# Kernel tuning notes

Measured on AMD Instinct MI355X. Metric: run time of the kernel, lower is better.

Reference implementation:

```python
import jax, jax.numpy as jnp
import numpy as np

N = 50000      # nodes
E = 800000     # edges
R = 8          # relation types
IN = 128       # in_dim
OUT = 128      # out_dim
H = 8          # num_heads
HD = OUT // H  # head dim = 16


def setup_inputs() -> dict:
    key = jax.random.key(0)
    ks = jax.random.split(key, 6)
    return {
        "h": jax.random.normal(ks[0], (N, IN), dtype=jnp.float32),
        "fc_weight": jax.random.normal(ks[1], (R, IN, OUT), dtype=jnp.float32) * 0.05,
        "attn_weight": jax.random.normal(ks[2], (R, H, 2 * HD), dtype=jnp.float32) * 0.05,
        "src": jax.random.randint(ks[3], (E,), 0, N, dtype=jnp.int32),
        "dst": jax.random.randint(ks[4], (E,), 0, N, dtype=jnp.int32),
        "etype": jax.random.randint(ks[5], (E,), 0, R, dtype=jnp.int32),
    }


def reference(h, fc_weight, attn_weight, src, dst, etype):
    # Per-relation projection of ALL node features (equivalent math to the
    # per-edge gathered bmm in the original, without materializing E x IN x OUT):
    # [R, N, OUT] -> [R, N, H, HD]
    z_nodes = jnp.einsum('ni,rio->rno', h, fc_weight).reshape(R, N, H, HD)
    z_s = z_nodes[etype, src]   # [E, H, HD]  (== bmm(h[src], fc_weight[etype]))
    z_d = z_nodes[etype, dst]   # [E, H, HD]
    aw = attn_weight[etype]     # [E, H, 2*HD]
    # a = sum(cat([z_s, z_d], -1) * attn_weight[etype], -1)
    a = jnp.sum(z_s * aw[:, :, :HD], axis=2) + jnp.sum(z_d * aw[:, :, HD:], axis=2)  # [E, H]
    e = jax.nn.leaky_relu(a)    # torch F.leaky_relu_ default slope 0.01

    # Edge softmax per destination node (per head), numerically stable.
    m = jax.ops.segment_max(e, dst, num_segments=N)          # [N, H]
    m = jnp.where(jnp.isfinite(m), m, jnp.zeros_like(m))     # guard empty nodes
    ex = jnp.exp(e - m[dst])                                 # [E, H]
    denom = jax.ops.segment_sum(ex, dst, num_segments=N)     # [N, H]
    num = jax.ops.segment_sum(ex[:, :, None] * z_s, dst, num_segments=N)  # [N, H, HD]
    out = num / jnp.maximum(denom, 1e-9)[:, :, None]         # [N, H, HD]
    return out
```

## Files before the change

kernel.cpp:

```cpp
#include <hip/hip_runtime.h>

#define NN 50000
#define NE 800000
#define NR 8
#define DIN 128
#define DOUT 128
#define NH 8

#define NB_SCAN ((NN + 255) / 256)

typedef __attribute__((ext_vector_type(8))) short bf16x8;
typedef __attribute__((ext_vector_type(4))) float f32x4;

__device__ __forceinline__ unsigned short f2bf(float f) {
  unsigned u = __float_as_uint(f);
  unsigned r = (u + 0x7FFFu + ((u >> 16) & 1u)) >> 16;
  return (unsigned short)r;
}
__device__ __forceinline__ float bf2f(unsigned short b) {
  return __uint_as_float(((unsigned)b) << 16);
}

__global__ __launch_bounds__(256) void prep_fcf(
    const float* __restrict__ fc, const float* __restrict__ attn,
    unsigned short* __restrict__ fcf) {
  int idx = blockIdx.x * 256 + threadIdx.x;
  if (idx >= NR * DIN * 144) return;
  int r = idx / (DIN * 144);
  int rem = idx - r * (DIN * 144);
  int k = rem / 144;
  int j = rem - k * 144;
  float v;
  if (j < DOUT) {
    v = fc[((size_t)r * DIN + k) * DOUT + j];
  } else {
    int cc = j - DOUT;
    int hh = cc & 7, p = cc >> 3;
    const float* fr = fc + ((size_t)r * DIN + k) * DOUT + hh * 16;
    const float* ar = attn + ((size_t)r * NH + hh) * 32 + p * 16;
    v = 0.f;
#pragma unroll
    for (int d = 0; d < 16; ++d) v += fr[d] * ar[d];
  }
  int t = j >> 4, c = j & 15, ks = k >> 5, gg = (k >> 3) & 3, i = k & 7;
  fcf[((((size_t)r * 9 + t) * 4 + ks) * 4 + gg) * 128 + c * 8 + i] = f2bf(v);
}

__global__ __launch_bounds__(256) void gemm_mfma(
    const float* __restrict__ h, const unsigned short* __restrict__ fcf,
    unsigned short* __restrict__ z, unsigned short* __restrict__ s_buf) {
  const int n0 = blockIdx.x * 64;
  const int rr0 = blockIdx.y * 4;
  const int w = threadIdx.x >> 6;
  const int lane = threadIdx.x & 63;
  const int g = lane >> 4, c = lane & 15;
  const int nbase = n0 + w * 16;

  __shared__ unsigned short zst[4][16][130];

  int arow = nbase + c;
  if (arow > NN - 1) arow = NN - 1;
  const float* ha = h + (size_t)arow * DIN + g * 8;
  bf16x8 af[4];
#pragma unroll
  for (int ks = 0; ks < 4; ++ks) {
    float4 v0 = *(const float4*)(ha + ks * 32);
    float4 v1 = *(const float4*)(ha + ks * 32 + 4);
    bf16x8 a;
    a[0] = (short)f2bf(v0.x); a[1] = (short)f2bf(v0.y);
    a[2] = (short)f2bf(v0.z); a[3] = (short)f2bf(v0.w);
    a[4] = (short)f2bf(v1.x); a[5] = (short)f2bf(v1.y);
    a[6] = (short)f2bf(v1.z); a[7] = (short)f2bf(v1.w);
    af[ks] = a;
  }

  const int node = nbase + c;

  for (int ri = 0; ri < 4; ++ri) {
    const int r = rr0 + ri;
    const unsigned short* fb = fcf + ((size_t)r * 36 * 64 + lane) * 8;
    f32x4 acc[9];
#pragma unroll
    for (int t = 0; t < 9; ++t) acc[t] = (f32x4){0.f, 0.f, 0.f, 0.f};

#pragma unroll
    for (int ks = 0; ks < 4; ++ks)
#pragma unroll
      for (int t = 0; t < 9; ++t) {
        bf16x8 bf = *(const bf16x8*)(fb + (size_t)(t * 4 + ks) * 512);
        acc[t] = __builtin_amdgcn_mfma_f32_16x16x32_bf16(bf, af[ks], acc[t], 0, 0, 0);
      }

#pragma unroll
    for (int t = 0; t < 8; ++t) {
      ushort4 wv;
      wv.x = f2bf(acc[t][0]); wv.y = f2bf(acc[t][1]);
      wv.z = f2bf(acc[t][2]); wv.w = f2bf(acc[t][3]);
      *(ushort4*)&zst[w][c][t * 16 + g * 4] = wv;
    }
    __builtin_amdgcn_s_waitcnt(0);
    unsigned short* zb = z + ((size_t)r * NN + nbase) * DOUT;
#pragma unroll
    for (int p = 0; p < 4; ++p) {
      int row = 4 * p + (lane >> 4);
      if (nbase + row < NN) {
        bf16x8 v = *(const bf16x8*)&zst[w][row][(lane & 15) * 8];
        *(bf16x8*)(zb + row * DOUT + (lane & 15) * 8) = v;
      }
    }

    if (node < NN) {
      ushort4 sv;
      sv.x = f2bf(acc[8][0]); sv.y = f2bf(acc[8][1]);
      sv.z = f2bf(acc[8][2]); sv.w = f2bf(acc[8][3]);
      *(ushort4*)&s_buf[((size_t)r * NN + node) * 16 + g * 4] = sv;
    }
  }
}

__global__ __launch_bounds__(256) void hist_kernel(const int* __restrict__ dst,
                                                   int* __restrict__ deg) {
  int e = blockIdx.x * blockDim.x + threadIdx.x;
  if (e < NE) atomicAdd(&deg[dst[e]], 1);
}

__global__ __launch_bounds__(256) void scan1(const int* __restrict__ deg,
                                             int* __restrict__ bsum) {
  __shared__ int ws_[4];
  int gi = blockIdx.x * 256 + threadIdx.x;
  int v = (gi < NN) ? deg[gi] : 0;
#pragma unroll
  for (int m = 1; m < 64; m <<= 1) v += __shfl_xor(v, m);
  if ((threadIdx.x & 63) == 0) ws_[threadIdx.x >> 6] = v;
  __syncthreads();
  if (threadIdx.x == 0) bsum[blockIdx.x] = ws_[0] + ws_[1] + ws_[2] + ws_[3];
}

__global__ __launch_bounds__(256) void scan2(const int* __restrict__ bsum,
                                             int* __restrict__ bbase,
                                             int* __restrict__ row_start) {
  __shared__ int part[256];
  int t = threadIdx.x;
  part[t] = (t < NB_SCAN) ? bsum[t] : 0;
  __syncthreads();
  for (int off = 1; off < 256; off <<= 1) {
    int v = (t >= off) ? part[t - off] : 0;
    __syncthreads();
    part[t] += v;
    __syncthreads();
  }
  if (t < NB_SCAN) bbase[t] = (t == 0) ? 0 : part[t - 1];
  if (t == 0) row_start[NN] = NE;
}

__global__ __launch_bounds__(256) void scan3(const int* __restrict__ deg,
                                             const int* __restrict__ bbase,
                                             int* __restrict__ row_start) {
  __shared__ int part[256];
  int t = threadIdx.x;
  int gi = blockIdx.x * 256 + t;
  int v = (gi < NN) ? deg[gi] : 0;
  part[t] = v;
  __syncthreads();
  for (int off = 1; off < 256; off <<= 1) {
    int x = (t >= off) ? part[t - off] : 0;
    __syncthreads();
    part[t] += x;
    __syncthreads();
  }
  if (gi < NN) row_start[gi] = bbase[blockIdx.x] + part[t] - v;
}

__global__ __launch_bounds__(256) void scatter_kernel(
    const int* __restrict__ src, const int* __restrict__ dst,
    const int* __restrict__ et, const unsigned short* __restrict__ s_buf,
    const int* __restrict__ row_start, int* __restrict__ cursor,
    unsigned short* __restrict__ es, unsigned* __restrict__ sidx) {
  int e = blockIdx.x * blockDim.x + threadIdx.x;
  if (e >= NE) return;
  int s = src[e], d = dst[e], r = et[e];
  int pos = row_start[d] + atomicAdd(&cursor[d], 1);
  ushort4 sa0 = *(const ushort4*)&s_buf[((size_t)r * NN + s) * 16];
  ushort4 sa1 = *(const ushort4*)&s_buf[((size_t)r * NN + s) * 16 + 4];
  ushort4 sb0 = *(const ushort4*)&s_buf[((size_t)r * NN + d) * 16 + 8];
  ushort4 sb1 = *(const ushort4*)&s_buf[((size_t)r * NN + d) * 16 + 12];
  float ev[8] = {bf2f(sa0.x) + bf2f(sb0.x), bf2f(sa0.y) + bf2f(sb0.y),
                 bf2f(sa0.z) + bf2f(sb0.z), bf2f(sa0.w) + bf2f(sb0.w),
                 bf2f(sa1.x) + bf2f(sb1.x), bf2f(sa1.y) + bf2f(sb1.y),
                 bf2f(sa1.z) + bf2f(sb1.z), bf2f(sa1.w) + bf2f(sb1.w)};
  ushort4 w0, w1;
  unsigned short wv[8];
#pragma unroll
  for (int hh = 0; hh < 8; ++hh) {
    float x = ev[hh];
    x = x > 0.f ? x : 0.01f * x;
    wv[hh] = f2bf(x);
  }
  w0.x = wv[0]; w0.y = wv[1]; w0.z = wv[2]; w0.w = wv[3];
  w1.x = wv[4]; w1.y = wv[5]; w1.z = wv[6]; w1.w = wv[7];
  *(ushort4*)&es[(size_t)pos * 8] = w0;
  *(ushort4*)&es[(size_t)pos * 8 + 4] = w1;
  sidx[pos] = (unsigned)s | ((unsigned)r << 16);
}

__global__ __launch_bounds__(256) void node_accum(
    const int* __restrict__ row_start, const unsigned short* __restrict__ es,
    const unsigned* __restrict__ sidx, const unsigned short* __restrict__ z,
    float* __restrict__ out) {
  int wave = threadIdx.x >> 6;
  int lane = threadIdx.x & 63;
  int n = blockIdx.x * 4 + wave;
  if (n >= NN) return;
  int b0 = row_start[n];
  int deg = row_start[n + 1] - b0;

  int hl = lane & 7;
  int jg = lane >> 3;
  int c16 = lane & 15;
  int e4 = lane >> 4;

  float maxv = -INFINITY;
  for (int j = jg; j < deg; j += 8)
    maxv = fmaxf(maxv, bf2f(es[(size_t)(b0 + j) * 8 + hl]));
#pragma unroll
  for (int m = 8; m < 64; m <<= 1) maxv = fmaxf(maxv, __shfl_xor(maxv, m));

  float acc[8] = {0.f, 0.f, 0.f, 0.f, 0.f, 0.f, 0.f, 0.f};
  float den = 0.f;
  int hh16 = c16 >> 1;

  for (int cch = 0; cch < deg; cch += 8) {
    int j = cch + jg;
    float ex = 0.f;
    if (j < deg) ex = __expf(bf2f(es[(size_t)(b0 + j) * 8 + hl]) - maxv);
    den += ex;
    int rem = min(8, deg - cch);
    unsigned pk = sidx[b0 + cch + min(lane & 7, rem - 1)];
#pragma unroll
    for (int half = 0; half < 2; ++half) {
      if (half * 4 >= rem) break;
      int o = half * 4 + e4;
      float exb = __shfl(ex, (o << 3) | hh16);
      unsigned p = __shfl(pk, o);
      unsigned sr_ = p & 0xFFFFu;
      unsigned rr = p >> 16;
      bf16x8 v = *(const bf16x8*)&z[(((size_t)rr * NN + sr_) << 7) + c16 * 8];
#pragma unroll
      for (int i = 0; i < 8; ++i)
        acc[i] += exb * bf2f((unsigned short)v[i]);
    }
  }
#pragma unroll
  for (int m = 8; m < 64; m <<= 1) den += __shfl_xor(den, m);
#pragma unroll
  for (int i = 0; i < 8; ++i) {
    acc[i] += __shfl_xor(acc[i], 16);
    acc[i] += __shfl_xor(acc[i], 32);
  }
  float deno = __shfl(den, hh16);
  float inv = 1.0f / fmaxf(deno, 1e-9f);
  if (lane < 16) {
    float* ob = out + ((size_t)n << 7) + lane * 8;
    *(float4*)ob = make_float4(acc[0] * inv, acc[1] * inv, acc[2] * inv, acc[3] * inv);
    *(float4*)(ob + 4) = make_float4(acc[4] * inv, acc[5] * inv, acc[6] * inv, acc[7] * inv);
  }
}

extern "C" void kernel_launch(void* const* d_in, const int* in_sizes, int n_in,
                              void* d_out, int out_size, void* d_ws, size_t ws_size,
                              hipStream_t stream) {
  const float* h = (const float*)d_in[0];
  const float* fc = (const float*)d_in[1];
  const float* attn = (const float*)d_in[2];
  const int* src = (const int*)d_in[3];
  const int* dst = (const int*)d_in[4];
  const int* et = (const int*)d_in[5];
  float* out = (float*)d_out;

  char* wsb = (char*)d_ws;
  size_t off = 0;
  unsigned short* z = (unsigned short*)(wsb + off);    off += (size_t)NR * NN * DOUT * 2;
  unsigned short* s_buf = (unsigned short*)(wsb + off);off += (size_t)NR * NN * 16 * 2;
  unsigned short* es = (unsigned short*)(wsb + off);   off += (size_t)NE * NH * 2;
  unsigned* sidx = (unsigned*)(wsb + off);             off += (size_t)NE * 4;
  unsigned short* fcf = (unsigned short*)(wsb + off);  off += (size_t)NR * 9 * 4 * 4 * 128 * 2;
  int* deg = (int*)(wsb + off);                        off += (size_t)NN * 4;
  int* row_start = (int*)(wsb + off);                  off += (size_t)(NN + 1) * 4;
  int* cursor = (int*)(wsb + off);                     off += (size_t)NN * 4;
  int* bsum = (int*)(wsb + off);                       off += (size_t)NB_SCAN * 4;
  int* bbase = (int*)(wsb + off);                      off += (size_t)NB_SCAN * 4;

  hipMemsetAsync(deg, 0, (size_t)NN * sizeof(int), stream);
  hipMemsetAsync(cursor, 0, (size_t)NN * sizeof(int), stream);

  prep_fcf<<<(NR * DIN * 144 + 255) / 256, 256, 0, stream>>>(fc, attn, fcf);

  dim3 ggrid((NN + 63) / 64, 2);
  gemm_mfma<<<ggrid, 256, 0, stream>>>(h, fcf, z, s_buf);

  hist_kernel<<<(NE + 255) / 256, 256, 0, stream>>>(dst, deg);
  scan1<<<NB_SCAN, 256, 0, stream>>>(deg, bsum);
  scan2<<<1, 256, 0, stream>>>(bsum, bbase, row_start);
  scan3<<<NB_SCAN, 256, 0, stream>>>(deg, bbase, row_start);

  scatter_kernel<<<(NE + 255) / 256, 256, 0, stream>>>(src, dst, et, s_buf,
                                                       row_start, cursor, es, sidx);

  node_accum<<<(NN + 3) / 4, 256, 0, stream>>>(row_start, es, sidx, z, out);
}
```

Before: 284.0 us.

## Fuse edge score computation into node accumulation with online softmax

Result: faster. 274.5 us (-3.3%).

```diff
diff --git a/kernel.cpp b/kernel.cpp
--- a/kernel.cpp
+++ b/kernel.cpp
@@ -173,39 +173,18 @@
 
 __global__ __launch_bounds__(256) void scatter_kernel(
     const int* __restrict__ src, const int* __restrict__ dst,
-    const int* __restrict__ et, const unsigned short* __restrict__ s_buf,
-    const int* __restrict__ row_start, int* __restrict__ cursor,
-    unsigned short* __restrict__ es, unsigned* __restrict__ sidx) {
+    const int* __restrict__ et, const int* __restrict__ row_start,
+    int* __restrict__ cursor, unsigned* __restrict__ sidx) {
   int e = blockIdx.x * blockDim.x + threadIdx.x;
   if (e >= NE) return;
-  int s = src[e], d = dst[e], r = et[e];
+  int d = dst[e];
   int pos = row_start[d] + atomicAdd(&cursor[d], 1);
-  ushort4 sa0 = *(const ushort4*)&s_buf[((size_t)r * NN + s) * 16];
-  ushort4 sa1 = *(const ushort4*)&s_buf[((size_t)r * NN + s) * 16 + 4];
-  ushort4 sb0 = *(const ushort4*)&s_buf[((size_t)r * NN + d) * 16 + 8];
-  ushort4 sb1 = *(const ushort4*)&s_buf[((size_t)r * NN + d) * 16 + 12];
-  float ev[8] = {bf2f(sa0.x) + bf2f(sb0.x), bf2f(sa0.y) + bf2f(sb0.y),
-                 bf2f(sa0.z) + bf2f(sb0.z), bf2f(sa0.w) + bf2f(sb0.w),
-                 bf2f(sa1.x) + bf2f(sb1.x), bf2f(sa1.y) + bf2f(sb1.y),
-                 bf2f(sa1.z) + bf2f(sb1.z), bf2f(sa1.w) + bf2f(sb1.w)};
-  ushort4 w0, w1;
-  unsigned short wv[8];
-#pragma unroll
-  for (int hh = 0; hh < 8; ++hh) {
-    float x = ev[hh];
-    x = x > 0.f ? x : 0.01f * x;
-    wv[hh] = f2bf(x);
-  }
-  w0.x = wv[0]; w0.y = wv[1]; w0.z = wv[2]; w0.w = wv[3];
-  w1.x = wv[4]; w1.y = wv[5]; w1.z = wv[6]; w1.w = wv[7];
-  *(ushort4*)&es[(size_t)pos * 8] = w0;
-  *(ushort4*)&es[(size_t)pos * 8 + 4] = w1;
-  sidx[pos] = (unsigned)s | ((unsigned)r << 16);
+  sidx[pos] = (unsigned)src[e] | ((unsigned)et[e] << 16);
 }
 
 __global__ __launch_bounds__(256) void node_accum(
-    const int* __restrict__ row_start, const unsigned short* __restrict__ es,
-    const unsigned* __restrict__ sidx, const unsigned short* __restrict__ z,
+    const int* __restrict__ row_start, const unsigned* __restrict__ sidx,
+    const unsigned short* __restrict__ s_buf, const unsigned short* __restrict__ z,
     float* __restrict__ out) {
   int wave = threadIdx.x >> 6;
   int lane = threadIdx.x & 63;
@@ -218,30 +197,51 @@
   int jg = lane >> 3;
   int c16 = lane & 15;
   int e4 = lane >> 4;
-
-  float maxv = -INFINITY;
-  for (int j = jg; j < deg; j += 8)
-    maxv = fmaxf(maxv, bf2f(es[(size_t)(b0 + j) * 8 + hl]));
-#pragma unroll
-  for (int m = 8; m < 64; m <<= 1) maxv = fmaxf(maxv, __shfl_xor(maxv, m));
-
+  int hh16 = c16 >> 1;
+
+  float srn[8];
+#pragma unroll
+  for (int r = 0; r < 8; ++r)
+    srn[r] = bf2f(s_buf[((size_t)r * NN + n) * 16 + 8 + hl]);
+
+  float m = -INFINITY;
+  float den = 0.f;
   float acc[8] = {0.f, 0.f, 0.f, 0.f, 0.f, 0.f, 0.f, 0.f};
-  float den = 0.f;
-  int hh16 = c16 >> 1;
 
   for (int cch = 0; cch < deg; cch += 8) {
     int j = cch + jg;
-    float ex = 0.f;
-    if (j < deg) ex = __expf(bf2f(es[(size_t)(b0 + j) * 8 + hl]) - maxv);
-    den += ex;
     int rem = min(8, deg - cch);
-    unsigned pk = sidx[b0 + cch + min(lane & 7, rem - 1)];
+    float ev = -INFINITY;
+    unsigned pj = 0;
+    if (j < deg) {
+      pj = sidx[b0 + j];
+      unsigned s = pj & 0xFFFFu, r = pj >> 16;
+      float sl = bf2f(s_buf[((size_t)r * NN + s) * 16 + hl]);
+      float x = sl + srn[r];
+      ev = x > 0.f ? x : 0.01f * x;
+    }
+    float cm = ev;
+    cm = fmaxf(cm, __shfl_xor(cm, 8));
+    cm = fmaxf(cm, __shfl_xor(cm, 16));
+    cm = fmaxf(cm, __shfl_xor(cm, 32));
+    float newm = fmaxf(m, cm);
+    float scale = __expf(m - newm);
+    float ex = __expf(ev - newm);
+    float sumex = ex;
+    sumex += __shfl_xor(sumex, 8);
+    sumex += __shfl_xor(sumex, 16);
+    sumex += __shfl_xor(sumex, 32);
+    den = den * scale + sumex;
+    m = newm;
+    float sc_acc = __shfl(scale, hh16);
+#pragma unroll
+    for (int i = 0; i < 8; ++i) acc[i] *= sc_acc;
 #pragma unroll
     for (int half = 0; half < 2; ++half) {
       if (half * 4 >= rem) break;
       int o = half * 4 + e4;
       float exb = __shfl(ex, (o << 3) | hh16);
-      unsigned p = __shfl(pk, o);
+      unsigned p = __shfl(pj, o << 3);
       unsigned sr_ = p & 0xFFFFu;
       unsigned rr = p >> 16;
       bf16x8 v = *(const bf16x8*)&z[(((size_t)rr * NN + sr_) << 7) + c16 * 8];
@@ -250,8 +250,6 @@
         acc[i] += exb * bf2f((unsigned short)v[i]);
     }
   }
-#pragma unroll
-  for (int m = 8; m < 64; m <<= 1) den += __shfl_xor(den, m);
 #pragma unroll
   for (int i = 0; i < 8; ++i) {
     acc[i] += __shfl_xor(acc[i], 16);
@@ -281,7 +279,6 @@
   size_t off = 0;
   unsigned short* z = (unsigned short*)(wsb + off);    off += (size_t)NR * NN * DOUT * 2;
   unsigned short* s_buf = (unsigned short*)(wsb + off);off += (size_t)NR * NN * 16 * 2;
-  unsigned short* es = (unsigned short*)(wsb + off);   off += (size_t)NE * NH * 2;
   unsigned* sidx = (unsigned*)(wsb + off);             off += (size_t)NE * 4;
   unsigned short* fcf = (unsigned short*)(wsb + off);  off += (size_t)NR * 9 * 4 * 4 * 128 * 2;
   int* deg = (int*)(wsb + off);                        off += (size_t)NN * 4;
@@ -303,8 +300,8 @@
   scan2<<<1, 256, 0, stream>>>(bsum, bbase, row_start);
   scan3<<<NB_SCAN, 256, 0, stream>>>(deg, bbase, row_start);
 
-  scatter_kernel<<<(NE + 255) / 256, 256, 0, stream>>>(src, dst, et, s_buf,
-                                                       row_start, cursor, es, sidx);
-
-  node_accum<<<(NN + 3) / 4, 256, 0, stream>>>(row_start, es, sidx, z, out);
-}
+  scatter_kernel<<<(NE + 255) / 256, 256, 0, stream>>>(src, dst, et, row_start,
+                                                       cursor, sidx);
+
+  node_accum<<<(NN + 3) / 4, 256, 0, stream>>>(row_start, sidx, s_buf, z, out);
+}
```
